# Optimization experiments

Hardware: AMD Instinct MI355X
Metric: run time of the kernel (lower is better)

Reference implementation:

```python
import jax, jax.numpy as jnp
import numpy as np

B, H, HD, E = 4, 32, 128, 4096
PAST = 2048
SB = int(0.1 * PAST)   # start_budget fixed at prefill
RB = int(0.1 * PAST)   # recent_budget fixed at prefill
MERGE = 32             # merge_budget inside local_cam_mask


def setup_inputs() -> dict:
    key = jax.random.key(0)
    ks = jax.random.split(key, 10)
    S = PAST + 1
    # attention_masks_next built at the previous decode step:
    # ones on sink tokens [0:SB+1] and the trailing recent window [PAST-RB:S]
    m = jnp.zeros((B * H, S), jnp.float32)
    m = m.at[:, :SB + 1].set(1.0)
    m = m.at[:, PAST - RB:].set(1.0)
    w = lambda k: jax.random.normal(k, (E, E), jnp.float32) * 0.02
    return {
        "hidden_states": jax.random.normal(ks[0], (B, 1, E), jnp.float32),
        "past_key": jax.random.normal(ks[1], (B, H, PAST, HD), jnp.float32),
        "past_value": jax.random.normal(ks[2], (B, H, PAST, HD), jnp.float32),
        "attention_mask": jnp.zeros((B, 1, 1, S), jnp.float32),
        "attn_masks_next": m[:, None, :],
        "previous_scores": jax.random.uniform(ks[3], (B * H, PAST), jnp.float32, 0.0, 2.0),
        "Wq": w(ks[4]), "bq": jnp.zeros((E,), jnp.float32),
        "Wk": w(ks[5]), "bk": jnp.zeros((E,), jnp.float32),
        "Wv": w(ks[6]), "bv": jnp.zeros((E,), jnp.float32),
        "Wo": w(ks[7]), "bo": jnp.zeros((E,), jnp.float32),
        "start_budget": SB,
        "recent_budget": RB,
    }


def reference(hidden_states, past_key, past_value, attention_mask, attn_masks_next,
              previous_scores, Wq, bq, Wk, bk, Wv, bv, Wo, bo,
              start_budget, recent_budget):
    B_, T, E_ = hidden_states.shape
    H_, hd = past_key.shape[1], past_key.shape[-1]
    scaling = hd ** -0.5
    # projections (torch Linear: x @ W^T + b); q pre-scaled as in the module
    q = (hidden_states @ Wq.T + bq) * scaling
    k_new = (hidden_states @ Wk.T + bk).reshape(B_, T, H_, hd).transpose(0, 2, 1, 3)
    v_new = (hidden_states @ Wv.T + bv).reshape(B_, T, H_, hd).transpose(0, 2, 1, 3)
    k = jnp.concatenate([past_key, k_new], axis=2)   # [B,H,S,hd]
    v = jnp.concatenate([past_value, v_new], axis=2)
    S = k.shape[2]
    q = q.reshape(B_, T, H_, hd).transpose(0, 2, 1, 3).reshape(B_ * H_, T, hd)
    k = k.reshape(B_ * H_, S, hd)
    v = v.reshape(B_ * H_, S, hd)
    aw = jnp.einsum('bth,bsh->bts', q, k)            # [B*H, T, S]
    fmin = jnp.finfo(aw.dtype).min
    aw = aw.reshape(B_, H_, T, S) + attention_mask
    aw = jnp.maximum(aw, fmin).reshape(B_ * H_, T, S)
    # CAM eviction mask from the previous step
    aw = aw * attn_masks_next + (1.0 - attn_masks_next) * fmin
    # local_cam_mask: merge the evicted token's value into the next MERGE slots
    ti = previous_scores.shape[-1]                   # == S-1
    mean_attn = jnp.mean(jnp.concatenate(
        [previous_scores[:, :start_budget], previous_scores[:, ti - recent_budget:ti]],
        axis=-1), axis=-1)                            # [B*H]
    merge_prob = previous_scores[:, ti - recent_budget] / mean_attn
    merge_mask = (merge_prob > 1.0).astype(v.dtype)
    score1 = v[:, ti - recent_budget, :] * merge_mask[:, None] / MERGE  # [B*H,hd]
    v = v.at[:, ti - recent_budget + 1: ti - recent_budget + MERGE + 1, :].add(score1[:, None, :])
    v = v.at[:, start_budget, :].multiply(0.99)
    aw = jax.nn.softmax(aw, axis=-1)
    # decode step (previous_scores is not None): pin the merge-sink column to 1
    aw = aw.at[:, :, start_budget].set(1.0)
    out = jnp.einsum('bts,bsh->bth', aw, v)          # [B*H, T, hd]
    out = out.reshape(B_, H_, T, hd).transpose(0, 2, 1, 3).reshape(B_, T, E_)
    return out @ Wo.T + bo
```

## Files before the change

### kernel.cpp

```cpp
#include <hip/hip_runtime.h>
#include <cstdint>
#include <cstddef>

#define FMIN_F (-3.402823466e38f)

__device__ __forceinline__ float wave_sum(float v) {
#pragma unroll
    for (int off = 32; off > 0; off >>= 1)
        v += __shfl_down(v, off, 64);
    return v;
}

template <int NMAT>
__global__ __launch_bounds__(256) void gemv_tw_kernel(
    const float* __restrict__ X,
    const float* __restrict__ W0, const float* __restrict__ B0,
    const float* __restrict__ W1, const float* __restrict__ B1,
    const float* __restrict__ W2, const float* __restrict__ B2,
    float scale0,
    float* __restrict__ Y)
{
    const int o     = blockIdx.x;
    const int batch = (o >> 3) & 3;
    const int cm    = (o >> 5) * 8 + (o & 7);
    const int mi    = (NMAT == 1) ? 0 : (cm >> 8);
    const int chunk = cm & 255;

    __shared__ float4 sX[1024];
    const int tid = threadIdx.x;
    const float4* X4 = (const float4*)X + (size_t)batch * 1024;
    for (int i = tid; i < 1024; i += 256) sX[i] = X4[i];
    __syncthreads();

    const int wave = tid >> 6;
    const int lane = tid & 63;
    const int r0   = chunk * 16 + wave * 4;

    const float* W  = (mi == 0) ? W0 : (mi == 1) ? W1 : W2;
    const float* Bs = (mi == 0) ? B0 : (mi == 1) ? B1 : B2;
    const float4* Wr0 = (const float4*)W + (size_t)(r0 + 0) * 1024;
    const float4* Wr1 = Wr0 + 1024;
    const float4* Wr2 = Wr0 + 2048;
    const float4* Wr3 = Wr0 + 3072;

    float acc0 = 0.f, acc1 = 0.f, acc2 = 0.f, acc3 = 0.f;

#pragma unroll 1
    for (int s = 0; s < 8; ++s) {
        const int p0 = s * 128 + lane;
        const int p1 = p0 + 64;
        const float4 wa0 = Wr0[p0], wb0 = Wr0[p1];
        const float4 wa1 = Wr1[p0], wb1 = Wr1[p1];
        const float4 wa2 = Wr2[p0], wb2 = Wr2[p1];
        const float4 wa3 = Wr3[p0], wb3 = Wr3[p1];
        const float4 x0 = sX[p0];
        const float4 x1 = sX[p1];
        acc0 += wa0.x * x0.x + wa0.y * x0.y + wa0.z * x0.z + wa0.w * x0.w
              + wb0.x * x1.x + wb0.y * x1.y + wb0.z * x1.z + wb0.w * x1.w;
        acc1 += wa1.x * x0.x + wa1.y * x0.y + wa1.z * x0.z + wa1.w * x0.w
              + wb1.x * x1.x + wb1.y * x1.y + wb1.z * x1.z + wb1.w * x1.w;
        acc2 += wa2.x * x0.x + wa2.y * x0.y + wa2.z * x0.z + wa2.w * x0.w
              + wb2.x * x1.x + wb2.y * x1.y + wb2.z * x1.z + wb2.w * x1.w;
        acc3 += wa3.x * x0.x + wa3.y * x0.y + wa3.z * x0.z + wa3.w * x0.w
              + wb3.x * x1.x + wb3.y * x1.y + wb3.z * x1.z + wb3.w * x1.w;
    }

    acc0 = wave_sum(acc0);
    acc1 = wave_sum(acc1);
    acc2 = wave_sum(acc2);
    acc3 = wave_sum(acc3);
    if (lane == 0) {
        float* y = Y + ((size_t)(mi * 4 + batch)) * 4096 + r0;
        const float sc = (mi == 0) ? scale0 : 1.0f;
        y[0] = (acc0 + Bs[r0 + 0]) * sc;
        y[1] = (acc1 + Bs[r0 + 1]) * sc;
        y[2] = (acc2 + Bs[r0 + 2]) * sc;
        y[3] = (acc3 + Bs[r0 + 3]) * sc;
    }
}

__global__ __launch_bounds__(256) void score_kernel(
    const float* __restrict__ qkv,
    const float* __restrict__ pk,
    const float* __restrict__ amask,
    const float* __restrict__ cam,
    const int* __restrict__ sbp, const int* __restrict__ rbp,
    float* __restrict__ scores)
{
    constexpr int PAST = 2048, S = 2049, HD = 128;
    const int bh = blockIdx.y;
    const int b  = bh >> 5;
    const int h  = bh & 31;
    const int SB = sbp[0], RB = rbp[0];
    const int NS = SB + 1;
    const int NA = NS + RB + 1;

    const int wave = threadIdx.x >> 6;
    const int lane = threadIdx.x & 63;

    const float* qh   = qkv + (size_t)b * 4096 + h * HD;
    const float* knew = qkv + (size_t)(4 + b) * 4096 + h * HD;
    const float2 ql = ((const float2*)qh)[lane];

#pragma unroll
    for (int j = 0; j < 8; ++j) {
        const int i = blockIdx.x * 32 + j * 4 + wave;
        if (i >= NA) continue;
        const int s = (i < NS) ? i : (PAST - RB + (i - NS));
        const float2* kr = (s < PAST)
            ? (const float2*)(pk + ((size_t)bh * PAST + s) * HD)
            : (const float2*)knew;
        const float2 kk = kr[lane];
        float p = ql.x * kk.x + ql.y * kk.y;
        p = wave_sum(p);
        if (lane == 0) {
            const float m  = cam[(size_t)bh * S + s];
            float sc = fmaxf(p + amask[(size_t)b * S + s], FMIN_F);
            sc = sc * m + (1.0f - m) * FMIN_F;
            scores[(size_t)bh * 512 + i] = sc;
        }
    }
}

__global__ __launch_bounds__(256) void softmax_kernel(
    const float* __restrict__ ps,
    const int* __restrict__ sbp, const int* __restrict__ rbp,
    float* __restrict__ scores)
{
    constexpr int PAST = 2048;
    const int bh = blockIdx.x;
    const int SB = sbp[0], RB = rbp[0];
    const int NS = SB + 1;
    const int NA = NS + RB + 1;
    const int tid = threadIdx.x;

    __shared__ float s_c[512];
    __shared__ float s_red[256];
    __shared__ float s_mm;

    for (int i = tid; i < NA; i += 256) s_c[i] = scores[(size_t)bh * 512 + i];

    {
        float part = 0.0f;
        const int cnt = SB + RB;
        for (int i = tid; i < cnt; i += 256) {
            const int idx = (i < SB) ? i : (PAST - RB + (i - SB));
            part += ps[(size_t)bh * PAST + idx];
        }
        s_red[tid] = part;
    }
    __syncthreads();
#pragma unroll
    for (int st = 128; st > 0; st >>= 1) {
        if (tid < st) s_red[tid] += s_red[tid + st];
        __syncthreads();
    }
    if (tid == 0) {
        const float mean = s_red[0] / (float)(SB + RB);
        const float prob = ps[(size_t)bh * PAST + (PAST - RB)] / mean;
        s_mm = (prob > 1.0f) ? (1.0f / 32.0f) : 0.0f;
    }
    __syncthreads();

    float mx = -INFINITY;
    for (int i = tid; i < NA; i += 256) mx = fmaxf(mx, s_c[i]);
    s_red[tid] = mx;
    __syncthreads();
#pragma unroll
    for (int st = 128; st > 0; st >>= 1) {
        if (tid < st) s_red[tid] = fmaxf(s_red[tid], s_red[tid + st]);
        __syncthreads();
    }
    const float gmax = s_red[0];
    __syncthreads();

    float lsum = 0.0f;
    for (int i = tid; i < NA; i += 256) {
        const float e = expf(s_c[i] - gmax);
        s_c[i] = e;
        lsum += e;
    }
    s_red[tid] = lsum;
    __syncthreads();
#pragma unroll
    for (int st = 128; st > 0; st >>= 1) {
        if (tid < st) s_red[tid] += s_red[tid + st];
        __syncthreads();
    }
    const float inv = 1.0f / s_red[0];
    __syncthreads();
    for (int i = tid; i < NA; i += 256) s_c[i] *= inv;
    __syncthreads();

    if (tid == 0) {
        float sm = 0.0f;
#pragma unroll
        for (int j = 1; j <= 32; ++j) sm += s_c[NS + j];
        s_c[NS] += s_mm * sm;
        s_c[SB]  = 0.99f;
    }
    __syncthreads();

    for (int i = tid; i < NA; i += 256) scores[(size_t)bh * 512 + i] = s_c[i];
}

__global__ __launch_bounds__(256) void pv_kernel(
    const float* __restrict__ qkv,
    const float* __restrict__ pv,
    const float* __restrict__ coeff,
    const int* __restrict__ sbp, const int* __restrict__ rbp,
    float* __restrict__ partial)
{
    constexpr int PAST = 2048, HD = 128;
    const int bh = blockIdx.y;
    const int b  = bh >> 5;
    const int h  = bh & 31;
    const int SB = sbp[0], RB = rbp[0];
    const int NS = SB + 1;
    const int NA = NS + RB + 1;
    const int CPC = (NA + 7) >> 3;
    const int i0 = blockIdx.x * CPC;
    const int i1 = min(NA, i0 + CPC);

    const int tid  = threadIdx.x;
    const int d    = tid & 127;
    const int half = tid >> 7;

    __shared__ float s_co[64];
    __shared__ float s_red[256];

    if (tid < i1 - i0) s_co[tid] = coeff[(size_t)bh * 512 + i0 + tid];
    __syncthreads();

    const float* vnew = qkv + (size_t)(8 + b) * 4096 + h * HD;

    float acc = 0.0f;
    for (int i = i0 + half; i < i1; i += 2) {
        const int s = (i < NS) ? i : (PAST - RB + (i - NS));
        const float* vr = (s < PAST)
            ? (pv + ((size_t)bh * PAST + s) * HD)
            : vnew;
        acc += s_co[i - i0] * vr[d];
    }
    s_red[tid] = acc;
    __syncthreads();
    if (tid < 128)
        partial[((size_t)bh * 8 + blockIdx.x) * HD + d] = s_red[tid] + s_red[tid + 128];
}

__global__ __launch_bounds__(256) void attn_reduce_kernel(
    const float* __restrict__ partial,
    float* __restrict__ attn_out)
{
    const int idx = blockIdx.x * 256 + threadIdx.x;
    const int bh = idx >> 7;
    const int d  = idx & 127;
    float s = 0.0f;
#pragma unroll
    for (int c = 0; c < 8; ++c)
        s += partial[(size_t)bh * 1024 + c * 128 + d];
    attn_out[idx] = s;
}

extern "C" void kernel_launch(void* const* d_in, const int* in_sizes, int n_in,
                              void* d_out, int out_size, void* d_ws, size_t ws_size,
                              hipStream_t stream)
{
    const float* hs = (const float*)d_in[0];
    const float* pk = (const float*)d_in[1];
    const float* pv = (const float*)d_in[2];
    const float* am = (const float*)d_in[3];
    const float* cm = (const float*)d_in[4];
    const float* ps = (const float*)d_in[5];
    const float* Wq = (const float*)d_in[6];
    const float* bq = (const float*)d_in[7];
    const float* Wk = (const float*)d_in[8];
    const float* bk = (const float*)d_in[9];
    const float* Wv = (const float*)d_in[10];
    const float* bv = (const float*)d_in[11];
    const float* Wo = (const float*)d_in[12];
    const float* bo = (const float*)d_in[13];
    const int*   sb = (const int*)d_in[14];
    const int*   rb = (const int*)d_in[15];

    float* qkv  = (float*)d_ws;
    float* aout = qkv + 3 * 4 * 4096;
    float* sc   = aout + 4 * 4096;
    float* part = sc + 128 * 512;
    float* out  = (float*)d_out;

    const float scaling = 0.08838834764831845f;

    gemv_tw_kernel<3><<<3072, 256, 0, stream>>>(hs, Wq, bq, Wk, bk, Wv, bv, scaling, qkv);

    score_kernel<<<dim3(16, 128), 256, 0, stream>>>(qkv, pk, am, cm, sb, rb, sc);
    softmax_kernel<<<128, 256, 0, stream>>>(ps, sb, rb, sc);
    pv_kernel<<<dim3(8, 128), 256, 0, stream>>>(qkv, pv, sc, sb, rb, part);
    attn_reduce_kernel<<<64, 256, 0, stream>>>(part, aout);

    gemv_tw_kernel<1><<<1024, 256, 0, stream>>>(aout, Wo, bo, Wo, bo, Wo, bo, 1.0f, out);
}
```

Measured before the change: 111.8 us.

## Stage GEMV weight tiles into LDS via async global_load_lds double buffering

Rewrites the projection GEMV so weights are copied directly from global memory into swizzled, double-buffered LDS tiles using the global_load_lds builtin, overlapping the next tile's load with the current tile's dot products. Work is redistributed so each wave covers 16 rows over a quarter of the columns, followed by shuffle and cross-wave LDS reductions. This aims to improve load pipelining and bandwidth on the memory-bound weight stream, at the cost of much larger shared memory per block (lower occupancy) and extra reduction/synchronisation.

After: 132.7 us. 18.7% more time.

```diff
diff --git a/kernel.cpp b/kernel.cpp
--- a/kernel.cpp
+++ b/kernel.cpp
@@ -11,8 +11,14 @@
     return v;
 }
 
+__device__ __forceinline__ void load16_to_lds(const float4* g, float4* l) {
+    __builtin_amdgcn_global_load_lds(
+        (const __attribute__((address_space(1))) void*)g,
+        (__attribute__((address_space(3))) void*)l, 16, 0, 0);
+}
+
 template <int NMAT>
-__global__ __launch_bounds__(256) void gemv_tw_kernel(
+__global__ __launch_bounds__(256) void gemv_gl_kernel(
     const float* __restrict__ X,
     const float* __restrict__ W0, const float* __restrict__ B0,
     const float* __restrict__ W1, const float* __restrict__ B1,
@@ -20,13 +26,15 @@
     float scale0,
     float* __restrict__ Y)
 {
+    __shared__ float4 sX[1024];
+    __shared__ float4 tiles[4][2][512];
+
     const int o     = blockIdx.x;
     const int batch = (o >> 3) & 3;
     const int cm    = (o >> 5) * 8 + (o & 7);
     const int mi    = (NMAT == 1) ? 0 : (cm >> 8);
     const int chunk = cm & 255;
 
-    __shared__ float4 sX[1024];
     const int tid = threadIdx.x;
     const float4* X4 = (const float4*)X + (size_t)batch * 1024;
     for (int i = tid; i < 1024; i += 256) sX[i] = X4[i];
@@ -34,48 +42,59 @@
 
     const int wave = tid >> 6;
     const int lane = tid & 63;
-    const int r0   = chunk * 16 + wave * 4;
+    const int row  = lane & 15;
+    const int c    = lane >> 4;
 
     const float* W  = (mi == 0) ? W0 : (mi == 1) ? W1 : W2;
     const float* Bs = (mi == 0) ? B0 : (mi == 1) ? B1 : B2;
-    const float4* Wr0 = (const float4*)W + (size_t)(r0 + 0) * 1024;
-    const float4* Wr1 = Wr0 + 1024;
-    const float4* Wr2 = Wr0 + 2048;
-    const float4* Wr3 = Wr0 + 3072;
-
-    float acc0 = 0.f, acc1 = 0.f, acc2 = 0.f, acc3 = 0.f;
-
+    const float4* W4 = (const float4*)W + (size_t)(chunk * 16) * 1024 + wave * 256;
+
+    float acc = 0.f;
+
+    auto stage = [&](int t, int p) {
+        float4* dst = &tiles[wave][p][0];
+#pragma unroll
+        for (int s = 0; s < 8; ++s) {
+            const int i  = s * 64 + lane;
+            const int rr = i >> 5;
+            const int cf = (i & 31) ^ (rr & 7);
+            load16_to_lds(W4 + (size_t)rr * 1024 + t * 32 + cf, dst + s * 64);
+        }
+    };
+    auto consume = [&](int t, int p) {
+        const float4* tb = &tiles[wave][p][0];
+#pragma unroll
+        for (int j = 0; j < 8; ++j) {
+            const int cf   = c * 8 + j;
+            const int slot = row * 32 + (cf ^ (row & 7));
+            const float4 w = tb[slot];
+            const float4 x = sX[wave * 256 + t * 32 + cf];
+            acc += w.x * x.x + w.y * x.y + w.z * x.z + w.w * x.w;
+        }
+    };
+
+    stage(0, 0);
+    asm volatile("s_waitcnt vmcnt(0)" ::: "memory");
 #pragma unroll 1
-    for (int s = 0; s < 8; ++s) {
-        const int p0 = s * 128 + lane;
-        const int p1 = p0 + 64;
-        const float4 wa0 = Wr0[p0], wb0 = Wr0[p1];
-        const float4 wa1 = Wr1[p0], wb1 = Wr1[p1];
-        const float4 wa2 = Wr2[p0], wb2 = Wr2[p1];
-        const float4 wa3 = Wr3[p0], wb3 = Wr3[p1];
-        const float4 x0 = sX[p0];
-        const float4 x1 = sX[p1];
-        acc0 += wa0.x * x0.x + wa0.y * x0.y + wa0.z * x0.z + wa0.w * x0.w
-              + wb0.x * x1.x + wb0.y * x1.y + wb0.z * x1.z + wb0.w * x1.w;
-        acc1 += wa1.x * x0.x + wa1.y * x0.y + wa1.z * x0.z + wa1.w * x0.w
-              + wb1.x * x1.x + wb1.y * x1.y + wb1.z * x1.z + wb1.w * x1.w;
-        acc2 += wa2.x * x0.x + wa2.y * x0.y + wa2.z * x0.z + wa2.w * x0.w
-              + wb2.x * x1.x + wb2.y * x1.y + wb2.z * x1.z + wb2.w * x1.w;
-        acc3 += wa3.x * x0.x + wa3.y * x0.y + wa3.z * x0.z + wa3.w * x0.w
-              + wb3.x * x1.x + wb3.y * x1.y + wb3.z * x1.z + wb3.w * x1.w;
-    }
-
-    acc0 = wave_sum(acc0);
-    acc1 = wave_sum(acc1);
-    acc2 = wave_sum(acc2);
-    acc3 = wave_sum(acc3);
-    if (lane == 0) {
-        float* y = Y + ((size_t)(mi * 4 + batch)) * 4096 + r0;
-        const float sc = (mi == 0) ? scale0 : 1.0f;
-        y[0] = (acc0 + Bs[r0 + 0]) * sc;
-        y[1] = (acc1 + Bs[r0 + 1]) * sc;
-        y[2] = (acc2 + Bs[r0 + 2]) * sc;
-        y[3] = (acc3 + Bs[r0 + 3]) * sc;
+    for (int t = 0; t < 8; ++t) {
+        if (t + 1 < 8) stage(t + 1, (t + 1) & 1);
+        consume(t, t & 1);
+        asm volatile("s_waitcnt vmcnt(0)" ::: "memory");
+    }
+
+    acc += __shfl_xor(acc, 16, 64);
+    acc += __shfl_xor(acc, 32, 64);
+
+    __syncthreads();
+    float* s_part = (float*)sX;
+    if (lane < 16) s_part[wave * 16 + row] = acc;
+    __syncthreads();
+    if (tid < 16) {
+        float s = s_part[tid] + s_part[16 + tid] + s_part[32 + tid] + s_part[48 + tid];
+        const int r = chunk * 16 + tid;
+        s += Bs[r];
+        if (mi == 0) s *= scale0;
+        Y[((size_t)(mi * 4 + batch)) * 4096 + r] = s;
     }
 }
 
@@ -291,12 +310,12 @@
 
     const float scaling = 0.08838834764831845f;
 
-    gemv_tw_kernel<3><<<3072, 256, 0, stream>>>(hs, Wq, bq, Wk, bk, Wv, bv, scaling, qkv);
+    gemv_gl_kernel<3><<<3072, 256, 0, stream>>>(hs, Wq, bq, Wk, bk, Wv, bv, scaling, qkv);
 
     score_kernel<<<dim3(16, 128), 256, 0, stream>>>(qkv, pk, am, cm, sb, rb, sc);
     softmax_kernel<<<128, 256, 0, stream>>>(ps, sb, rb, sc);
     pv_kernel<<<dim3(8, 128), 256, 0, stream>>>(qkv, pv, sc, sb, rb, part);
     attn_reduce_kernel<<<64, 256, 0, stream>>>(part, aout);
 
-    gemv_tw_kernel<1><<<1024, 256, 0, stream>>>(aout, Wo, bo, Wo, bo, Wo, bo, 1.0f, out);
-}
+    gemv_gl_kernel<1><<<1024, 256, 0, stream>>>(aout, Wo, bo, Wo, bo, Wo, bo, 1.0f, out);
+}
```
